# Kernel optimization log

Measured on AMD Instinct MI355X. Metric: run time of the kernel, lower is better.

Reference implementation:

```python
import jax, jax.numpy as jnp
import numpy as np

B, N, FIN, HID, HEADS, LAYERS = 2048, 62, 128, 512, 8, 3
FOUT = HID // HEADS  # 64


def setup_inputs() -> dict:
    key = jax.random.key(0)
    ks = jax.random.split(key, 12)
    x = jax.random.normal(ks[0], (B, N, FIN), dtype=jnp.float32)
    adj = jax.random.randint(ks[1], (B, N, N), 0, 2, dtype=jnp.int32)
    # BatchNorm1d(62) params (eval mode, running stats)
    bn_gamma = jax.random.normal(ks[2], (N,), dtype=jnp.float32) * 0.1 + 1.0
    bn_beta = jax.random.normal(ks[3], (N,), dtype=jnp.float32) * 0.1
    bn_mean = jax.random.normal(ks[4], (N,), dtype=jnp.float32) * 0.1
    bn_var = jax.random.uniform(ks[5], (N,), dtype=jnp.float32, minval=0.5, maxval=1.5)
    # input MLP
    W_mlp = jax.random.normal(ks[6], (FIN, HID), dtype=jnp.float32) / np.sqrt(FIN)
    b_mlp = jnp.zeros((HID,), dtype=jnp.float32)
    # GAT params: one W [HID, FOUT] and one a [2*FOUT] per (layer, head)
    W_gat = jax.random.normal(ks[7], (LAYERS, HEADS, HID, FOUT), dtype=jnp.float32) / np.sqrt(HID)
    a_gat = jax.random.normal(ks[8], (LAYERS, HEADS, 2 * FOUT), dtype=jnp.float32) / np.sqrt(2 * FOUT)
    # output head
    W_out = jax.random.normal(ks[9], (HID, 3), dtype=jnp.float32) / np.sqrt(HID)
    b_out = jnp.zeros((3,), dtype=jnp.float32)
    return {
        "x": x, "adj": adj,
        "bn_gamma": bn_gamma, "bn_beta": bn_beta, "bn_mean": bn_mean, "bn_var": bn_var,
        "W_mlp": W_mlp, "b_mlp": b_mlp,
        "W_gat": W_gat, "a_gat": a_gat,
        "W_out": W_out, "b_out": b_out,
    }


def reference(x, adj, bn_gamma, bn_beta, bn_mean, bn_var, W_mlp, b_mlp, W_gat, a_gat, W_out, b_out):
    eps = 1e-5
    alpha = 0.2  # LeakyReLU slope
    # BatchNorm1d over the node dim (C=62), eval mode
    xb = (x - bn_mean[None, :, None]) * (bn_gamma / jnp.sqrt(bn_var + eps))[None, :, None] + bn_beta[None, :, None]
    h_x = xb @ W_mlp + b_mlp  # [B, N, HID]
    mask = adj > 0  # [B, N, N]
    n_layers, n_heads, _, f_out = W_gat.shape
    for l in range(n_layers):
        # all heads at once: h [H, B, N, FOUT]
        h = jnp.einsum('bnf,hfd->hbnd', h_x, W_gat[l])
        a1 = a_gat[l][:, :f_out]   # multiplies the repeat(1,N,1) part -> h_j
        a2 = a_gat[l][:, f_out:]   # multiplies the repeat(1,1,N) part -> h_i
        f1 = jnp.einsum('hbnd,hd->hbn', h, a1)  # per-node source term
        f2 = jnp.einsum('hbnd,hd->hbn', h, a2)  # per-node dest term
        # e[h,b,i,j] = leaky(a2.h_i + a1.h_j)  (matches cat/repeat layout)
        e = jax.nn.leaky_relu(f2[:, :, :, None] + f1[:, :, None, :], alpha)
        e = jnp.where(mask[None], e, jnp.float32(-9e15))
        # torch F.softmax(attention, dim=1) on [B,N,N] -> axis=2 here (the i axis)
        att = jax.nn.softmax(e, axis=2)
        hp = jnp.einsum('hbij,hbjd->hbid', att, h)
        hp = jax.nn.elu(hp)
        # concat heads on feature dim -> [B, N, HID]
        h_x = jnp.transpose(hp, (1, 2, 0, 3)).reshape(h_x.shape[0], h_x.shape[1], n_heads * f_out)
    pooled = jnp.sum(h_x, axis=1)  # [B, HID]
    logits = pooled @ W_out + b_out  # [B, 3]
    return jax.nn.log_softmax(logits, axis=-1)
```

## Files before the change

### kernel.cpp

```cpp
#include <hip/hip_runtime.h>
#include <cstdint>
#include <cstddef>

#define B_ 2048
#define N_ 62
#define FIN_ 128
#define HID_ 512
#define HEADS_ 8
#define FOUT_ 64
#define LAYERS_ 3
#define M_ (B_*N_)

typedef __bf16 bf16x8 __attribute__((ext_vector_type(8)));
typedef __bf16 bf16x4 __attribute__((ext_vector_type(4)));
typedef float  f32x4  __attribute__((ext_vector_type(4)));
typedef unsigned short u16;

#define LOG2E 1.4426950408889634f

#if __has_builtin(__builtin_amdgcn_exp2f)
#define EXP2F(x) __builtin_amdgcn_exp2f(x)
#else
#define EXP2F(x) exp2f(x)
#endif
#if __has_builtin(__builtin_amdgcn_logf)
#define LOG2F(x) __builtin_amdgcn_logf(x)
#else
#define LOG2F(x) log2f(x)
#endif

static __device__ __forceinline__ u16 f2bf(float f) {
    union { float f; uint32_t u; } v; v.f = f;
    uint32_t u = v.u;
    return (u16)((u + 0x7fffu + ((u >> 16) & 1u)) >> 16);
}
static __device__ __forceinline__ float bf2f(u16 s) {
    union { uint32_t u; float f; } v; v.u = ((uint32_t)s) << 16;
    return v.f;
}
static __device__ __forceinline__ float rdlane(float v, int l) {
    union { float f; int i; } a, b; a.f = v;
    b.i = __builtin_amdgcn_readlane(a.i, l);
    return b.f;
}
static __device__ __forceinline__ bf16x4 pack4(f32x4 v) {
    bf16x4 o;
    o[0] = (__bf16)v[0]; o[1] = (__bf16)v[1];
    o[2] = (__bf16)v[2]; o[3] = (__bf16)v[3];
    return o;
}

__global__ __launch_bounds__(256) void repack_w(
    const float* __restrict__ Wm, const float* __restrict__ Wg,
    const float* __restrict__ ag,
    u16* __restrict__ wmlp_t, u16* __restrict__ wgat2)
{
    int idx = blockIdx.x * 256 + threadIdx.x;
    const int T1 = HID_ * FIN_;
    const int T2 = LAYERS_ * HEADS_ * 80 * HID_;
    if (idx < T1) {
        int n = idx / FIN_, k = idx % FIN_;
        wmlp_t[idx] = f2bf(Wm[k * HID_ + n]);
    } else if (idx < T1 + T2) {
        int j = idx - T1;
        int lh = j / (80 * HID_);
        int r  = j % (80 * HID_);
        int n = r / HID_, k = r % HID_;
        float v;
        if (n < 64) {
            v = Wg[((size_t)lh * HID_ + k) * FOUT_ + n];
        } else if (n < 66) {
            const float* ap = ag + (size_t)lh * 128 + (n - 64) * 64;
            const float* wrow = Wg + ((size_t)lh * HID_ + k) * FOUT_;
            float s = 0.f;
            for (int d = 0; d < 64; d++) s += wrow[d] * ap[d];
            v = s * LOG2E;
        } else {
            v = 0.f;
        }
        wgat2[j] = f2bf(v);
    }
}

__global__ __launch_bounds__(256) void build_masks(
    const int* __restrict__ adj, uint64_t* __restrict__ masks,
    uint64_t* __restrict__ masksT)
{
    __shared__ uint32_t m32[128];
    const int b = blockIdx.x, tid = threadIdx.x;
    if (tid < 128) m32[tid] = 0;
    __syncthreads();
    const int* a = adj + (size_t)b * N_ * N_;
    for (int idx = tid; idx < N_ * N_; idx += 256) {
        int i = idx / N_, j = idx % N_;
        if (a[idx] > 0) atomicOr(&m32[i * 2 + (j >> 5)], 1u << (j & 31));
    }
    __syncthreads();
    if (tid < 128) ((uint32_t*)(masks + (size_t)b * 64))[tid] = m32[tid];
    if (tid < 64) {
        int j = tid;
        uint64_t c = 0;
        for (int i = 0; i < N_; i++) {
            uint64_t bit = (m32[i * 2 + (j >> 5)] >> (j & 31)) & 1u;
            c |= bit << i;
        }
        masksT[(size_t)b * 64 + j] = c;
    }
}

#define S_R  72
#define RSZ  4608
#define S_X  136
#define X0   27648

__global__ __launch_bounds__(512, 4) void gat_fused(
    const float* __restrict__ x,
    const float* __restrict__ bng, const float* __restrict__ bnb,
    const float* __restrict__ bnm, const float* __restrict__ bnv,
    const u16* __restrict__ wmlp_t, const float* __restrict__ bm,
    const u16* __restrict__ wgat2,
    const uint64_t* __restrict__ masks, const uint64_t* __restrict__ masksT,
    const float* __restrict__ Wout, const float* __restrict__ bout,
    float* __restrict__ out)
{
    __shared__ __align__(16) u16 buf[36864];
    __shared__ uint64_t msk[64];
    __shared__ __align__(16) float fstat[1544];
    float* F1 = fstat;
    float* F2 = fstat + 512;
    float* LS = fstat + 1024;

    const int tid = threadIdx.x, b = blockIdx.x;
    const int wave = tid >> 6, lane = tid & 63;
    const int lr = lane & 15, lq = lane >> 4;
    const int w64 = wave * 64;
    const int wreg = wave * RSZ;

    const uint64_t cm = masksT[(size_t)b * 64 + lane];
    const uint32_t cml = (uint32_t)cm, cmh = (uint32_t)(cm >> 32);

    {
        const float* xg = x + (size_t)b * N_ * FIN_;
        for (int idx = tid; idx < 2048; idx += 512) {
            int n = idx >> 5, kq = idx & 31;
            bf16x4 o = {(__bf16)0.f, (__bf16)0.f, (__bf16)0.f, (__bf16)0.f};
            if (n < N_) {
                float s = bng[n] * rsqrtf(bnv[n] + 1e-5f);
                float sh = bnb[n] - bnm[n] * s;
                float4 v = *(const float4*)(xg + n * FIN_ + kq * 4);
                o[0] = (__bf16)(v.x * s + sh); o[1] = (__bf16)(v.y * s + sh);
                o[2] = (__bf16)(v.z * s + sh); o[3] = (__bf16)(v.w * s + sh);
            }
            *(bf16x4*)&buf[X0 + n * S_X + kq * 4] = o;
        }
        if (tid < 64) msk[tid] = (tid < N_) ? masks[(size_t)b * 64 + tid] : 0ull;
    }
    __syncthreads();

    {
        f32x4 acc[4][4];
#pragma unroll
        for (int mt = 0; mt < 4; mt++)
#pragma unroll
            for (int nt = 0; nt < 4; nt++) acc[mt][nt] = (f32x4){0.f, 0.f, 0.f, 0.f};
        const int c0 = w64;
#pragma unroll
        for (int kt = 0; kt < 4; kt++) {
            int k0 = kt * 32;
            bf16x8 xf[4];
#pragma unroll
            for (int nt = 0; nt < 4; nt++)
                xf[nt] = *(const bf16x8*)&buf[X0 + (nt * 16 + lr) * S_X + k0 + lq * 8];
#pragma unroll
            for (int mt = 0; mt < 4; mt++) {
                bf16x8 wf = *(const bf16x8*)(wmlp_t + (size_t)(c0 + mt * 16 + lr) * FIN_ + k0 + lq * 8);
#pragma unroll
                for (int nt = 0; nt < 4; nt++)
                    acc[mt][nt] = __builtin_amdgcn_mfma_f32_16x16x32_bf16(
                        wf, xf[nt], acc[mt][nt], 0, 0, 0);
            }
        }
        __syncthreads();
        f32x4 bl[4];
#pragma unroll
        for (int mt = 0; mt < 4; mt++)
            bl[mt] = *(const f32x4*)&bm[c0 + mt * 16 + lq * 4];
#pragma unroll
        for (int mt = 0; mt < 4; mt++)
#pragma unroll
            for (int nt = 0; nt < 4; nt++) {
                int node = nt * 16 + lr;
                if (node < N_)
                    *(bf16x4*)&buf[wreg + node * S_R + mt * 16 + lq * 4] =
                        pack4(acc[mt][nt] + bl[mt]);
            }
        if (lane < 16) {
            uint4 z = {0u, 0u, 0u, 0u};
            *(uint4*)&buf[wreg + (N_ + (lane >> 3)) * S_R + (lane & 7) * 8] = z;
        }
    }
    __syncthreads();

#pragma unroll 1
    for (int l = 0; l < LAYERS_; l++) {
        const u16* wp = wgat2 + (size_t)(l * HEADS_ + wave) * 80 * HID_;

        {
            f32x4 accf[4];
#pragma unroll
            for (int mt = 0; mt < 4; mt++) accf[mt] = (f32x4){0.f, 0.f, 0.f, 0.f};
#pragma unroll 4
            for (int kt = 0; kt < 16; kt++) {
                int koff = (kt >> 1) * RSZ + (kt & 1) * 32 + lq * 8;
                bf16x8 bfr = *(const bf16x8*)(wp + (size_t)(64 + lr) * HID_ + kt * 32 + lq * 8);
#pragma unroll
                for (int mt = 0; mt < 4; mt++) {
                    bf16x8 af = *(const bf16x8*)&buf[koff + (mt * 16 + lr) * S_R];
                    accf[mt] = __builtin_amdgcn_mfma_f32_16x16x32_bf16(
                        af, bfr, accf[mt], 0, 0, 0);
                }
            }
            if (lr < 2) {
                float* Fp = lr ? F2 : F1;
#pragma unroll
                for (int mt = 0; mt < 4; mt++)
#pragma unroll
                    for (int r = 0; r < 4; r++)
                        Fp[w64 + mt * 16 + lq * 4 + r] = accf[mt][r];
            }
        }

        {
            float p1 = F1[w64 + lane];
            float p2 = F2[w64 + lane];
            float pm = (lane < N_) ? p2 : -3.0e38f;
#pragma unroll
            for (int off = 32; off; off >>= 1) pm = fmaxf(pm, __shfl_xor(pm, off, 64));
            float vm = pm + p1;
            float m = fmaxf(vm, 0.2f * vm);
            float s0 = 0.f, s1 = 0.f;
#pragma unroll
            for (int i = 0; i < N_; i += 2) {
                float fa = rdlane(p2, i), fb = rdlane(p2, i + 1);
                float va = fa + p1, vb = fb + p1;
                va = fmaxf(va, 0.2f * va); vb = fmaxf(vb, 0.2f * vb);
                float ea = EXP2F(va - m), eb = EXP2F(vb - m);
                uint32_t w = (i < 32) ? cml : cmh;
                s0 += ((w >> (i & 31)) & 1u) ? ea : 0.f;
                s1 += ((w >> ((i + 1) & 31)) & 1u) ? eb : 0.f;
            }
            float ssum = fmaxf(s0 + s1, 1e-35f);
            LS[w64 + lane] = m + LOG2F(ssum);
        }

        f32x4 acc[4][4];
#pragma unroll
        for (int mt = 0; mt < 4; mt++)
#pragma unroll
            for (int nt = 0; nt < 4; nt++) acc[mt][nt] = (f32x4){0.f, 0.f, 0.f, 0.f};
#pragma unroll 4
        for (int kt = 0; kt < 16; kt++) {
            int koff = (kt >> 1) * RSZ + (kt & 1) * 32 + lq * 8;
            bf16x8 af[4];
#pragma unroll
            for (int mt = 0; mt < 4; mt++)
                af[mt] = *(const bf16x8*)&buf[koff + (mt * 16 + lr) * S_R];
#pragma unroll
            for (int nt = 0; nt < 4; nt++) {
                bf16x8 bfr = *(const bf16x8*)(wp + (size_t)(nt * 16 + lr) * HID_ + kt * 32 + lq * 8);
#pragma unroll
                for (int mt = 0; mt < 4; mt++)
                    acc[mt][nt] = __builtin_amdgcn_mfma_f32_16x16x32_bf16(
                        af[mt], bfr, acc[mt][nt], 0, 0, 0);
            }
        }

        __syncthreads();

#pragma unroll
        for (int mt = 0; mt < 4; mt++)
#pragma unroll
            for (int nt = 0; nt < 4; nt++)
                *(bf16x4*)&buf[wreg + (nt * 16 + lr) * S_R + mt * 16 + lq * 4] =
                    pack4(acc[mt][nt]);

        f32x4 acc2[4][4];
#pragma unroll
        for (int mt = 0; mt < 4; mt++)
#pragma unroll
            for (int it = 0; it < 4; it++) acc2[mt][it] = (f32x4){0.f, 0.f, 0.f, 0.f};
        float f2v[4];
#pragma unroll
        for (int it = 0; it < 4; it++) f2v[it] = F2[w64 + it * 16 + lr];
#pragma unroll
        for (int kt = 0; kt < 2; kt++) {
            int j0 = kt * 32 + lq * 8;
            bf16x8 pf[4];
#pragma unroll
            for (int h = 0; h < 2; h++) {
                f32x4 f1h = *(const f32x4*)&F1[w64 + j0 + 4 * h];
                f32x4 lsh = *(const f32x4*)&LS[w64 + j0 + 4 * h];
#pragma unroll
                for (int it = 0; it < 4; it++) {
                    uint64_t mi = msk[it * 16 + lr];
                    uint32_t sh = ((uint32_t)(mi >> (kt * 32))) >> (lq * 8 + 4 * h);
#pragma unroll
                    for (int t = 0; t < 4; t++) {
                        float v = f2v[it] + f1h[t];
                        v = fmaxf(v, 0.2f * v);
                        float p = EXP2F(v - lsh[t]);
                        p = ((sh >> t) & 1u) ? p : 0.f;
                        pf[it][4 * h + t] = (__bf16)p;
                    }
                }
            }
#pragma unroll
            for (int mt = 0; mt < 4; mt++) {
                bf16x8 ha = *(const bf16x8*)&buf[wreg + (mt * 16 + lr) * S_R + kt * 32 + lq * 8];
#pragma unroll
                for (int it = 0; it < 4; it++)
                    acc2[mt][it] = __builtin_amdgcn_mfma_f32_16x16x32_bf16(
                        ha, pf[it], acc2[mt][it], 0, 0, 0);
            }
        }

#pragma unroll
        for (int mt = 0; mt < 4; mt++)
#pragma unroll
            for (int it = 0; it < 4; it++) {
                int i = it * 16 + lr;
                f32x4 e;
#pragma unroll
                for (int r = 0; r < 4; r++) {
                    float v = acc2[mt][it][r];
                    e[r] = v > 0.f ? v : EXP2F(v * LOG2E) - 1.f;
                }
                if (i < N_)
                    *(bf16x4*)&buf[wreg + i * S_R + mt * 16 + lq * 4] = pack4(e);
            }
        if (lane < 16) {
            uint4 z = {0u, 0u, 0u, 0u};
            *(uint4*)&buf[wreg + (N_ + (lane >> 3)) * S_R + (lane & 7) * 8] = z;
        }
        __syncthreads();
    }

    {
        float s = 0.f;
#pragma unroll 2
        for (int n = 0; n < N_; n++)
            s += bf2f(buf[(tid >> 6) * RSZ + n * S_R + (tid & 63)]);
        fstat[tid] = s;
    }
    __syncthreads();
    if (tid < 192) {
        int c = tid >> 6, ln = tid & 63;
        float p = 0.f;
#pragma unroll
        for (int k = ln; k < HID_; k += 64) p += fstat[k] * Wout[k * 3 + c];
        for (int off = 32; off > 0; off >>= 1) p += __shfl_down(p, off, 64);
        if (ln == 0) fstat[1536 + c] = p + bout[c];
    }
    __syncthreads();
    if (tid == 0) {
        float l0 = fstat[1536], l1 = fstat[1537], l2 = fstat[1538];
        float mm = fmaxf(l0, fmaxf(l1, l2));
        float s = __expf(l0 - mm) + __expf(l1 - mm) + __expf(l2 - mm);
        float ls = mm + logf(s);
        out[b * 3 + 0] = l0 - ls;
        out[b * 3 + 1] = l1 - ls;
        out[b * 3 + 2] = l2 - ls;
    }
}

extern "C" void kernel_launch(void* const* d_in, const int* in_sizes, int n_in,
                              void* d_out, int out_size, void* d_ws, size_t ws_size,
                              hipStream_t stream)
{
    const float* x   = (const float*)d_in[0];
    const int*   adj = (const int*)d_in[1];
    const float* bng = (const float*)d_in[2];
    const float* bnb = (const float*)d_in[3];
    const float* bnm = (const float*)d_in[4];
    const float* bnv = (const float*)d_in[5];
    const float* Wm  = (const float*)d_in[6];
    const float* bm  = (const float*)d_in[7];
    const float* Wg  = (const float*)d_in[8];
    const float* ag  = (const float*)d_in[9];
    const float* Wo  = (const float*)d_in[10];
    const float* bo  = (const float*)d_in[11];
    float* out = (float*)d_out;

    uint64_t* masks  = (uint64_t*)d_ws;
    uint64_t* masksT = masks + (size_t)B_ * 64;
    u16* wmlp_t = (u16*)(masksT + (size_t)B_ * 64);
    u16* wgat2  = wmlp_t + (size_t)HID_ * FIN_;

    int rep_total = HID_ * FIN_ + LAYERS_ * HEADS_ * 80 * HID_;
    repack_w<<<(rep_total + 255) / 256, 256, 0, stream>>>(Wm, Wg, ag, wmlp_t, wgat2);
    build_masks<<<B_, 256, 0, stream>>>(adj, masks, masksT);

    gat_fused<<<B_, 512, 0, stream>>>(
        x, bng, bnb, bnm, bnv, wmlp_t, bm, wgat2,
        masks, masksT, Wo, bo, out);
}
```

Before: 727.8 us.

## Compute attention scores from projected features instead of extra folded-weight GEMM

Removes the separate 16-column MFMA pass that computed f1/f2 through weight columns with the attention vectors folded in. Instead, the main per-head projection GEMM runs first, and f1/f2 are obtained by dotting its fp32 accumulators with the attention vectors, followed by a butterfly shuffle reduction. This drops one pass over the hidden state in LDS and over global weights per layer, and shrinks the repacked weight buffer. In exchange it adds shuffle work, keeps the large accumulator array live across the softmax-statistics phase (more register pressure), and sets several loops to unroll 1.

```diff
diff --git a/kernel.cpp b/kernel.cpp
--- a/kernel.cpp
+++ b/kernel.cpp
@@ -52,33 +52,20 @@
 
 __global__ __launch_bounds__(256) void repack_w(
     const float* __restrict__ Wm, const float* __restrict__ Wg,
-    const float* __restrict__ ag,
     u16* __restrict__ wmlp_t, u16* __restrict__ wgat2)
 {
     int idx = blockIdx.x * 256 + threadIdx.x;
     const int T1 = HID_ * FIN_;
-    const int T2 = LAYERS_ * HEADS_ * 80 * HID_;
+    const int T2 = LAYERS_ * HEADS_ * 64 * HID_;
     if (idx < T1) {
         int n = idx / FIN_, k = idx % FIN_;
         wmlp_t[idx] = f2bf(Wm[k * HID_ + n]);
     } else if (idx < T1 + T2) {
         int j = idx - T1;
-        int lh = j / (80 * HID_);
-        int r  = j % (80 * HID_);
+        int lh = j / (64 * HID_);
+        int r  = j % (64 * HID_);
         int n = r / HID_, k = r % HID_;
-        float v;
-        if (n < 64) {
-            v = Wg[((size_t)lh * HID_ + k) * FOUT_ + n];
-        } else if (n < 66) {
-            const float* ap = ag + (size_t)lh * 128 + (n - 64) * 64;
-            const float* wrow = Wg + ((size_t)lh * HID_ + k) * FOUT_;
-            float s = 0.f;
-            for (int d = 0; d < 64; d++) s += wrow[d] * ap[d];
-            v = s * LOG2E;
-        } else {
-            v = 0.f;
-        }
-        wgat2[j] = f2bf(v);
+        wgat2[j] = f2bf(Wg[((size_t)lh * HID_ + k) * FOUT_ + n]);
     }
 }
 
@@ -118,7 +105,7 @@
     const float* __restrict__ bng, const float* __restrict__ bnb,
     const float* __restrict__ bnm, const float* __restrict__ bnv,
     const u16* __restrict__ wmlp_t, const float* __restrict__ bm,
-    const u16* __restrict__ wgat2,
+    const u16* __restrict__ wgat2, const float* __restrict__ ag,
     const uint64_t* __restrict__ masks, const uint64_t* __restrict__ masksT,
     const float* __restrict__ Wout, const float* __restrict__ bout,
     float* __restrict__ out)
@@ -164,7 +151,7 @@
 #pragma unroll
             for (int nt = 0; nt < 4; nt++) acc[mt][nt] = (f32x4){0.f, 0.f, 0.f, 0.f};
         const int c0 = w64;
-#pragma unroll
+#pragma unroll 1
         for (int kt = 0; kt < 4; kt++) {
             int k0 = kt * 32;
             bf16x8 xf[4];
@@ -203,32 +190,101 @@
 
 #pragma unroll 1
     for (int l = 0; l < LAYERS_; l++) {
-        const u16* wp = wgat2 + (size_t)(l * HEADS_ + wave) * 80 * HID_;
+        const u16* wp = wgat2 + (size_t)(l * HEADS_ + wave) * 64 * HID_;
+
+        f32x4 acc[4][4];
+#pragma unroll
+        for (int mt = 0; mt < 4; mt++)
+#pragma unroll
+            for (int nt = 0; nt < 4; nt++) acc[mt][nt] = (f32x4){0.f, 0.f, 0.f, 0.f};
+#pragma unroll 1
+        for (int kt = 0; kt < 16; kt++) {
+            int koff = (kt >> 1) * RSZ + (kt & 1) * 32 + lq * 8;
+            bf16x8 af[4];
+#pragma unroll
+            for (int mt = 0; mt < 4; mt++)
+                af[mt] = *(const bf16x8*)&buf[koff + (mt * 16 + lr) * S_R];
+#pragma unroll
+            for (int nt = 0; nt < 4; nt++) {
+                bf16x8 bfr = *(const bf16x8*)(wp + (size_t)(nt * 16 + lr) * HID_ + kt * 32 + lq * 8);
+#pragma unroll
+                for (int mt = 0; mt < 4; mt++)
+                    acc[mt][nt] = __builtin_amdgcn_mfma_f32_16x16x32_bf16(
+                        af[mt], bfr, acc[mt][nt], 0, 0, 0);
+            }
+        }
 
         {
-            f32x4 accf[4];
-#pragma unroll
-            for (int mt = 0; mt < 4; mt++) accf[mt] = (f32x4){0.f, 0.f, 0.f, 0.f};
-#pragma unroll 4
-            for (int kt = 0; kt < 16; kt++) {
-                int koff = (kt >> 1) * RSZ + (kt & 1) * 32 + lq * 8;
-                bf16x8 bfr = *(const bf16x8*)(wp + (size_t)(64 + lr) * HID_ + kt * 32 + lq * 8);
-#pragma unroll
-                for (int mt = 0; mt < 4; mt++) {
-                    bf16x8 af = *(const bf16x8*)&buf[koff + (mt * 16 + lr) * S_R];
-                    accf[mt] = __builtin_amdgcn_mfma_f32_16x16x32_bf16(
-                        af, bfr, accf[mt], 0, 0, 0);
+            float a1v[4], a2v[4];
+            const float* agl = ag + (size_t)(l * HEADS_ + wave) * 128;
+#pragma unroll
+            for (int nt = 0; nt < 4; nt++) {
+                a1v[nt] = agl[nt * 16 + lr] * LOG2E;
+                a2v[nt] = agl[64 + nt * 16 + lr] * LOG2E;
+            }
+            float p1v[16], p2v[16];
+#pragma unroll
+            for (int mt = 0; mt < 4; mt++)
+#pragma unroll
+                for (int r = 0; r < 4; r++) {
+                    float s1 = 0.f, s2 = 0.f;
+#pragma unroll
+                    for (int nt = 0; nt < 4; nt++) {
+                        float hv = acc[mt][nt][r];
+                        s1 = fmaf(hv, a1v[nt], s1);
+                        s2 = fmaf(hv, a2v[nt], s2);
+                    }
+                    p1v[mt * 4 + r] = s1;
+                    p2v[mt * 4 + r] = s2;
                 }
-            }
-            if (lr < 2) {
-                float* Fp = lr ? F2 : F1;
-#pragma unroll
-                for (int mt = 0; mt < 4; mt++)
-#pragma unroll
-                    for (int r = 0; r < 4; r++)
-                        Fp[w64 + mt * 16 + lq * 4 + r] = accf[mt][r];
-            }
-        }
+#pragma unroll
+            for (int c = 0; c < 8; c++) {
+                float tA = __shfl_xor(p1v[c], 8, 64);
+                float tB = __shfl_xor(p1v[c + 8], 8, 64);
+                p1v[c] = (lr & 8) ? (p1v[c + 8] + tB) : (p1v[c] + tA);
+                float uA = __shfl_xor(p2v[c], 8, 64);
+                float uB = __shfl_xor(p2v[c + 8], 8, 64);
+                p2v[c] = (lr & 8) ? (p2v[c + 8] + uB) : (p2v[c] + uA);
+            }
+#pragma unroll
+            for (int c = 0; c < 4; c++) {
+                float tA = __shfl_xor(p1v[c], 4, 64);
+                float tB = __shfl_xor(p1v[c + 4], 4, 64);
+                p1v[c] = (lr & 4) ? (p1v[c + 4] + tB) : (p1v[c] + tA);
+                float uA = __shfl_xor(p2v[c], 4, 64);
+                float uB = __shfl_xor(p2v[c + 4], 4, 64);
+                p2v[c] = (lr & 4) ? (p2v[c + 4] + uB) : (p2v[c] + uA);
+            }
+#pragma unroll
+            for (int c = 0; c < 2; c++) {
+                float tA = __shfl_xor(p1v[c], 2, 64);
+                float tB = __shfl_xor(p1v[c + 2], 2, 64);
+                p1v[c] = (lr & 2) ? (p1v[c + 2] + tB) : (p1v[c] + tA);
+                float uA = __shfl_xor(p2v[c], 2, 64);
+                float uB = __shfl_xor(p2v[c + 2], 2, 64);
+                p2v[c] = (lr & 2) ? (p2v[c + 2] + uB) : (p2v[c] + uA);
+            }
+            {
+                float tA = __shfl_xor(p1v[0], 1, 64);
+                float tB = __shfl_xor(p1v[1], 1, 64);
+                float f1fin = (lr & 1) ? (p1v[1] + tB) : (p1v[0] + tA);
+                float uA = __shfl_xor(p2v[0], 1, 64);
+                float uB = __shfl_xor(p2v[1], 1, 64);
+                float f2fin = (lr & 1) ? (p2v[1] + uB) : (p2v[0] + uA);
+                int node = (lr >> 2) * 16 + lq * 4 + (lr & 3);
+                F1[w64 + node] = f1fin;
+                F2[w64 + node] = f2fin;
+            }
+        }
+
+        __syncthreads();
+
+#pragma unroll
+        for (int mt = 0; mt < 4; mt++)
+#pragma unroll
+            for (int nt = 0; nt < 4; nt++)
+                *(bf16x4*)&buf[wreg + (nt * 16 + lr) * S_R + mt * 16 + lq * 4] =
+                    pack4(acc[mt][nt]);
 
         {
             float p1 = F1[w64 + lane];
@@ -252,37 +308,6 @@
             float ssum = fmaxf(s0 + s1, 1e-35f);
             LS[w64 + lane] = m + LOG2F(ssum);
         }
-
-        f32x4 acc[4][4];
-#pragma unroll
-        for (int mt = 0; mt < 4; mt++)
-#pragma unroll
-            for (int nt = 0; nt < 4; nt++) acc[mt][nt] = (f32x4){0.f, 0.f, 0.f, 0.f};
-#pragma unroll 4
-        for (int kt = 0; kt < 16; kt++) {
-            int koff = (kt >> 1) * RSZ + (kt & 1) * 32 + lq * 8;
-            bf16x8 af[4];
-#pragma unroll
-            for (int mt = 0; mt < 4; mt++)
-                af[mt] = *(const bf16x8*)&buf[koff + (mt * 16 + lr) * S_R];
-#pragma unroll
-            for (int nt = 0; nt < 4; nt++) {
-                bf16x8 bfr = *(const bf16x8*)(wp + (size_t)(nt * 16 + lr) * HID_ + kt * 32 + lq * 8);
-#pragma unroll
-                for (int mt = 0; mt < 4; mt++)
-                    acc[mt][nt] = __builtin_amdgcn_mfma_f32_16x16x32_bf16(
-                        af[mt], bfr, acc[mt][nt], 0, 0, 0);
-            }
-        }
-
-        __syncthreads();
-
-#pragma unroll
-        for (int mt = 0; mt < 4; mt++)
-#pragma unroll
-            for (int nt = 0; nt < 4; nt++)
-                *(bf16x4*)&buf[wreg + (nt * 16 + lr) * S_R + mt * 16 + lq * 4] =
-                    pack4(acc[mt][nt]);
 
         f32x4 acc2[4][4];
 #pragma unroll
@@ -396,11 +421,11 @@
     u16* wmlp_t = (u16*)(masksT + (size_t)B_ * 64);
     u16* wgat2  = wmlp_t + (size_t)HID_ * FIN_;
 
-    int rep_total = HID_ * FIN_ + LAYERS_ * HEADS_ * 80 * HID_;
-    repack_w<<<(rep_total + 255) / 256, 256, 0, stream>>>(Wm, Wg, ag, wmlp_t, wgat2);
+    int rep_total = HID_ * FIN_ + LAYERS_ * HEADS_ * 64 * HID_;
+    repack_w<<<(rep_total + 255) / 256, 256, 0, stream>>>(Wm, Wg, wmlp_t, wgat2);
     build_masks<<<B_, 256, 0, stream>>>(adj, masks, masksT);
 
     gat_fused<<<B_, 512, 0, stream>>>(
-        x, bng, bnb, bnm, bnv, wmlp_t, bm, wgat2,
+        x, bng, bnb, bnm, bnv, wmlp_t, bm, wgat2, ag,
         masks, masksT, Wo, bo, out);
 }
```

Measured after the change: 622.5 us. 14.5% less time.
